# Kernel tuning notes

Measured on AMD Instinct MI355X. Metric: run time of the kernel, lower is better.

## Reference

```python
import jax, jax.numpy as jnp
import numpy as np

ATT = 512  # attention_size

def setup_inputs() -> dict:
    key = jax.random.key(0)
    k0, k1, k2, k3, k4 = jax.random.split(key, 5)
    B, Sq, Sk, Din, Dmem = 32, 1024, 1024, 512, 512
    inputs = jax.random.normal(k0, (B, Sq, Din), dtype=jnp.float32)
    memory = jax.random.normal(k1, (B, Sk, Dmem), dtype=jnp.float32)
    memory_mask = jax.random.randint(k2, (B, Sk), 0, 2).astype(jnp.int32)
    W_input = (jax.random.normal(k3, (Din, ATT), dtype=jnp.float32) * 0.02)
    W_memory = (jax.random.normal(k4, (Dmem, ATT), dtype=jnp.float32) * 0.02)
    return {"inputs": inputs, "memory": memory, "memory_mask": memory_mask,
            "W_input": W_input, "W_memory": W_memory}

def reference(inputs, memory, memory_mask, W_input, W_memory):
    # projections (bias=False) + ReLU; dropout=0 -> identity
    x = jax.nn.relu(jnp.einsum('bqd,da->bqa', inputs, W_input))   # [B,Sq,A]
    m = jax.nn.relu(jnp.einsum('bkd,da->bka', memory, W_memory))  # [B,Sk,A]
    scale = 1.0 / jnp.sqrt(jnp.asarray(ATT, dtype=inputs.dtype))
    logits = jnp.einsum('bqa,bka->bqk', x, m) * scale             # [B,Sq,Sk]
    mask = (memory_mask[:, None, :] != 0)                         # [B,1,Sk] broadcast over Sq
    logits = jnp.where(mask, logits, jnp.asarray(-1e30, dtype=logits.dtype))
    score = jax.nn.softmax(logits, axis=-1)
    context = jnp.einsum('bqk,bkd->bqd', score, memory)           # [B,Sq,Dmem]
    return jnp.concatenate([context, inputs], axis=-1)            # [B,Sq,Dmem+Din]
```

## Files before the change

### kernel.cpp

```cpp
#include <hip/hip_runtime.h>

typedef __bf16 bf16x8 __attribute__((ext_vector_type(8)));
typedef float f32x4 __attribute__((ext_vector_type(4)));

__device__ __forceinline__ unsigned short f2bf(float f) {
    union { float f; unsigned u; } v; v.f = f;
    unsigned r = v.u + 0x7FFFu + ((v.u >> 16) & 1u);
    return (unsigned short)(r >> 16);
}

__global__ __launch_bounds__(256) void transpose_to_bf16(
    const float* __restrict__ src, unsigned short* __restrict__ dst,
    unsigned short* __restrict__ dst_copy, int S, int D)
{
    __shared__ float tile[32][33];
    const float* sb = src + (size_t)blockIdx.z * S * D;
    unsigned short* db = dst + (size_t)blockIdx.z * S * D;
    const int s0 = blockIdx.x * 32, d0 = blockIdx.y * 32;
    const int t = threadIdx.x;
    const int tr = t >> 5, tc = t & 31;
#pragma unroll
    for (int i = 0; i < 4; i++) {
        int s = s0 + tr + i * 8;
        float v = sb[(size_t)s * D + d0 + tc];
        tile[tr + i * 8][tc] = v;
        if (dst_copy)
            dst_copy[(size_t)blockIdx.z * S * D + (size_t)s * D + d0 + tc] = f2bf(v);
    }
    __syncthreads();
#pragma unroll
    for (int i = 0; i < 4; i++) {
        int d = d0 + tr + i * 8;
        db[(size_t)d * S + s0 + tc] = f2bf(tile[tc][tr + i * 8]);
    }
}

__global__ __launch_bounds__(256) void fuse_inputs_kernel(
    const float4* __restrict__ in, uint2* __restrict__ in_bf16, float4* __restrict__ out)
{
    int i = blockIdx.x * 256 + threadIdx.x;
    int bq = i >> 7;
    int d  = i & 127;
    float4 v = in[i];
    out[(size_t)bq * 256 + 128 + d] = v;
    union { unsigned short u[4]; uint2 p; } pk;
    pk.u[0] = f2bf(v.x); pk.u[1] = f2bf(v.y);
    pk.u[2] = f2bf(v.z); pk.u[3] = f2bf(v.w);
    in_bf16[i] = pk.p;
}

template<int CMODE>
__global__ __launch_bounds__(256, 2) void gemm_bt(
    const unsigned short* __restrict__ A, const unsigned short* __restrict__ Bt,
    void* __restrict__ Cptr, int K, float scale,
    const int* __restrict__ maskp, float* __restrict__ rowsum,
    long long aStride, long long bStride, long long cStride, int ldc)
{
    __shared__ __align__(16) unsigned short As[128 * 32];
    __shared__ __align__(16) unsigned short Bs[128 * 32];

    const int t = threadIdx.x;
    const int lane = t & 63;
    const int wave = t >> 6;
    const int z = blockIdx.z;

    const unsigned short* Ab = A + (size_t)z * aStride;
    const unsigned short* Bb = Bt + (size_t)z * bStride;

    const int rowA = blockIdx.y * 128;
    const int rowB = blockIdx.x * 128;

    f32x4 acc[4][4];
#pragma unroll
    for (int i = 0; i < 4; i++)
#pragma unroll
        for (int j = 0; j < 4; j++) acc[i][j] = f32x4{0.f, 0.f, 0.f, 0.f};

    const int wm = (wave >> 1) * 64;
    const int wn = (wave & 1) * 64;
    const int lrow = lane & 15;
    const int lk = (lane >> 4) * 8;

    const int sr = lane >> 2;
    const int skk = (lane & 3) * 8;
    const int c0 = wave, c1 = wave + 4;

    for (int kt = 0; kt < K; kt += 32) {
        const unsigned short* gb0 = Bb + (size_t)(rowB + c0 * 16 + sr) * K + kt + skk;
        const unsigned short* gb1 = Bb + (size_t)(rowB + c1 * 16 + sr) * K + kt + skk;
        __builtin_amdgcn_global_load_lds((const __attribute__((address_space(1))) void*)gb0,
                                         (__attribute__((address_space(3))) void*)&Bs[c0 * 512], 16, 0, 0);
        __builtin_amdgcn_global_load_lds((const __attribute__((address_space(1))) void*)gb1,
                                         (__attribute__((address_space(3))) void*)&Bs[c1 * 512], 16, 0, 0);
        const unsigned short* ga0 = Ab + (size_t)(rowA + c0 * 16 + sr) * K + kt + skk;
        const unsigned short* ga1 = Ab + (size_t)(rowA + c1 * 16 + sr) * K + kt + skk;
        __builtin_amdgcn_global_load_lds((const __attribute__((address_space(1))) void*)ga0,
                                         (__attribute__((address_space(3))) void*)&As[c0 * 512], 16, 0, 0);
        __builtin_amdgcn_global_load_lds((const __attribute__((address_space(1))) void*)ga1,
                                         (__attribute__((address_space(3))) void*)&As[c1 * 512], 16, 0, 0);
        __syncthreads();

        bf16x8 a[4], b[4];
#pragma unroll
        for (int i = 0; i < 4; i++) a[i] = *(const bf16x8*)&As[(wm + i * 16 + lrow) * 32 + lk];
#pragma unroll
        for (int j = 0; j < 4; j++) b[j] = *(const bf16x8*)&Bs[(wn + j * 16 + lrow) * 32 + lk];
#pragma unroll
        for (int i = 0; i < 4; i++)
#pragma unroll
            for (int j = 0; j < 4; j++)
                acc[i][j] = __builtin_amdgcn_mfma_f32_16x16x32_bf16(a[i], b[j], acc[i][j], 0, 0, 0);
        __syncthreads();
    }

    const int orow = (lane >> 4) * 4;
    const int ocol = lane & 15;

    if constexpr (CMODE == 0) {
        unsigned short* C = (unsigned short*)Cptr + (size_t)z * cStride;
#pragma unroll
        for (int i = 0; i < 4; i++)
#pragma unroll
            for (int j = 0; j < 4; j++) {
                int col = rowB + wn + j * 16 + ocol;
#pragma unroll
                for (int r = 0; r < 4; r++) {
                    int rw = rowA + wm + i * 16 + orow + r;
                    C[(size_t)rw * ldc + col] = f2bf(fmaxf(acc[i][j][r], 0.f));
                }
            }
    } else if constexpr (CMODE == 1) {
        unsigned short* C = (unsigned short*)Cptr + (size_t)z * cStride;
        const int* mk = maskp + (size_t)z * 1024;
        float* rs = rowsum + (size_t)z * 1024;
        int mv[4];
#pragma unroll
        for (int j = 0; j < 4; j++) mv[j] = mk[rowB + wn + j * 16 + ocol];
#pragma unroll
        for (int i = 0; i < 4; i++) {
            float part[4] = {0.f, 0.f, 0.f, 0.f};
#pragma unroll
            for (int j = 0; j < 4; j++) {
                int col = rowB + wn + j * 16 + ocol;
#pragma unroll
                for (int r = 0; r < 4; r++) {
                    float p = mv[j] ? __expf(acc[i][j][r] * scale) : 0.f;
                    part[r] += p;
                    int rw = rowA + wm + i * 16 + orow + r;
                    C[(size_t)rw * ldc + col] = f2bf(p);
                }
            }
#pragma unroll
            for (int r = 0; r < 4; r++) {
                float s = part[r];
                s += __shfl_xor(s, 1, 64);
                s += __shfl_xor(s, 2, 64);
                s += __shfl_xor(s, 4, 64);
                s += __shfl_xor(s, 8, 64);
                if (ocol == 0) atomicAdd(&rs[rowA + wm + i * 16 + orow + r], s);
            }
        }
    } else {
        float* C = (float*)Cptr + (size_t)z * cStride;
        const float* rs = rowsum + (size_t)z * 1024;
#pragma unroll
        for (int i = 0; i < 4; i++) {
            float inv[4];
#pragma unroll
            for (int r = 0; r < 4; r++)
                inv[r] = 1.0f / rs[rowA + wm + i * 16 + orow + r];
#pragma unroll
            for (int j = 0; j < 4; j++) {
                int col = rowB + wn + j * 16 + ocol;
#pragma unroll
                for (int r = 0; r < 4; r++) {
                    int rw = rowA + wm + i * 16 + orow + r;
                    C[(size_t)rw * ldc + col] = acc[i][j][r] * inv[r];
                }
            }
        }
    }
}

extern "C" void kernel_launch(void* const* d_in, const int* in_sizes, int n_in,
                              void* d_out, int out_size, void* d_ws, size_t ws_size,
                              hipStream_t stream)
{
    const float* inputs = (const float*)d_in[0];
    const float* memory = (const float*)d_in[1];
    const int*   mmask  = (const int*)d_in[2];
    const float* W_in   = (const float*)d_in[3];
    const float* W_mem  = (const float*)d_in[4];
    float* out = (float*)d_out;

    char* ws = (char*)d_ws;
    const unsigned long long MB = 1048576ull;
    unsigned short* Wt_in  = (unsigned short*)(ws);
    unsigned short* Wt_mem = (unsigned short*)(ws + 524288);
    unsigned short* InB16  = (unsigned short*)(ws + 1 * MB);
    unsigned short* MemB16 = (unsigned short*)(ws + 1 * MB + 32 * MB);
    unsigned short* P      = (unsigned short*)(ws + 1 * MB);
    unsigned short* MemT   = (unsigned short*)(ws + 1 * MB + 64 * MB);
    unsigned short* Xq     = (unsigned short*)(ws + 1 * MB + 96 * MB);
    unsigned short* Xm     = (unsigned short*)(ws + 1 * MB + 128 * MB);
    float*          rowsum = (float*)(ws + 1 * MB + 160 * MB);

    const float scale = 0.04419417382415922f;

    transpose_to_bf16<<<dim3(16, 16, 1), 256, 0, stream>>>(W_in,  Wt_in,  nullptr, 512, 512);
    transpose_to_bf16<<<dim3(16, 16, 1), 256, 0, stream>>>(W_mem, Wt_mem, nullptr, 512, 512);
    transpose_to_bf16<<<dim3(32, 16, 32), 256, 0, stream>>>(memory, MemT, MemB16, 1024, 512);

    fuse_inputs_kernel<<<16384, 256, 0, stream>>>(
        (const float4*)inputs, (uint2*)InB16, (float4*)out);

    hipMemsetAsync(rowsum, 0, 32 * 1024 * sizeof(float), stream);

    gemm_bt<0><<<dim3(4, 256, 1), 256, 0, stream>>>(
        InB16, Wt_in, Xq, 512, 0.f, nullptr, nullptr, 0, 0, 0, 512);
    gemm_bt<0><<<dim3(4, 256, 1), 256, 0, stream>>>(
        MemB16, Wt_mem, Xm, 512, 0.f, nullptr, nullptr, 0, 0, 0, 512);

    gemm_bt<1><<<dim3(8, 8, 32), 256, 0, stream>>>(
        Xq, Xm, P, 512, scale, mmask, rowsum, 1024ll * 512, 1024ll * 512, 1024ll * 1024, 1024);

    gemm_bt<2><<<dim3(4, 8, 32), 256, 0, stream>>>(
        P, MemT, out, 1024, 1.f, nullptr, rowsum, 1024ll * 1024, 512ll * 1024, 1024ll * 1024, 1024);
}
```

Before: 454.2 us.

## Compact unmasked memory keys and skip masked work in attention GEMMs

Adds a per-batch prefix scan over the memory mask that builds a compacted list of valid key indices and a count padded to 128. Memory rows are gathered into compacted bf16 and transposed buffers, so the memory projection, the QK logits GEMM and the PV GEMM only cover the valid keys, with early exits for tiles past the padded count and a dynamic K in the final GEMM. About half the keys are masked, so roughly half the attention and memory-projection FLOPs go away. The cost is an extra scan launch and a gather with indirect reads.

```diff
diff --git a/kernel.cpp b/kernel.cpp
--- a/kernel.cpp
+++ b/kernel.cpp
@@ -9,29 +9,82 @@
     return (unsigned short)(r >> 16);
 }
 
-__global__ __launch_bounds__(256) void transpose_to_bf16(
-    const float* __restrict__ src, unsigned short* __restrict__ dst,
-    unsigned short* __restrict__ dst_copy, int S, int D)
+__global__ __launch_bounds__(256) void mask_scan_kernel(
+    const int* __restrict__ mask, int* __restrict__ kidx,
+    int* __restrict__ cnt, int* __restrict__ padded)
+{
+    const int b = blockIdx.x;
+    const int* m = mask + b * 1024;
+    const int t = threadIdx.x;
+    int v[4]; int s = 0;
+#pragma unroll
+    for (int e = 0; e < 4; e++) { v[e] = (m[t * 4 + e] != 0) ? 1 : 0; s += v[e]; }
+    const int lane = t & 63, wv = t >> 6;
+    int x = s;
+#pragma unroll
+    for (int off = 1; off < 64; off <<= 1) {
+        int y = __shfl_up(x, off, 64);
+        if (lane >= off) x += y;
+    }
+    __shared__ int wsum[4];
+    if (lane == 63) wsum[wv] = x;
+    __syncthreads();
+    int base = 0;
+    for (int w = 0; w < wv; w++) base += wsum[w];
+    int pos = base + x - s;
+#pragma unroll
+    for (int e = 0; e < 4; e++)
+        if (v[e]) kidx[b * 1024 + pos++] = t * 4 + e;
+    if (t == 255) {
+        int total = base + x;
+        cnt[b] = total;
+        padded[b] = (total + 127) & ~127;
+    }
+}
+
+__global__ __launch_bounds__(256) void transpose_w_kernel(
+    const float* __restrict__ W0, const float* __restrict__ W1,
+    unsigned short* __restrict__ D0, unsigned short* __restrict__ D1)
 {
     __shared__ float tile[32][33];
-    const float* sb = src + (size_t)blockIdx.z * S * D;
-    unsigned short* db = dst + (size_t)blockIdx.z * S * D;
+    const float* src = blockIdx.z ? W1 : W0;
+    unsigned short* dst = blockIdx.z ? D1 : D0;
     const int s0 = blockIdx.x * 32, d0 = blockIdx.y * 32;
-    const int t = threadIdx.x;
-    const int tr = t >> 5, tc = t & 31;
+    const int t = threadIdx.x, tr = t >> 5, tc = t & 31;
+#pragma unroll
+    for (int i = 0; i < 4; i++)
+        tile[tr + i * 8][tc] = src[(size_t)(s0 + tr + i * 8) * 512 + d0 + tc];
+    __syncthreads();
+#pragma unroll
+    for (int i = 0; i < 4; i++)
+        dst[(size_t)(d0 + tr + i * 8) * 512 + s0 + tc] = f2bf(tile[tc][tr + i * 8]);
+}
+
+__global__ __launch_bounds__(256) void gather_mem_kernel(
+    const float* __restrict__ memory, const int* __restrict__ kidx,
+    const int* __restrict__ cnt, const int* __restrict__ padded,
+    unsigned short* __restrict__ MemG, unsigned short* __restrict__ MemGT)
+{
+    const int b = blockIdx.z;
+    const int j0 = blockIdx.x * 32, d0 = blockIdx.y * 32;
+    if (j0 >= padded[b]) return;
+    const int nb = cnt[b];
+    __shared__ float tile[32][33];
+    const float* src = memory + (size_t)b * 1024 * 512;
+    const int t = threadIdx.x, tr = t >> 5, tc = t & 31;
 #pragma unroll
     for (int i = 0; i < 4; i++) {
-        int s = s0 + tr + i * 8;
-        float v = sb[(size_t)s * D + d0 + tc];
+        int j = j0 + tr + i * 8;
+        float v = 0.f;
+        if (j < nb) v = src[(size_t)kidx[b * 1024 + j] * 512 + d0 + tc];
         tile[tr + i * 8][tc] = v;
-        if (dst_copy)
-            dst_copy[(size_t)blockIdx.z * S * D + (size_t)s * D + d0 + tc] = f2bf(v);
+        MemG[(size_t)b * 1024 * 512 + (size_t)j * 512 + d0 + tc] = f2bf(v);
     }
     __syncthreads();
 #pragma unroll
     for (int i = 0; i < 4; i++) {
         int d = d0 + tr + i * 8;
-        db[(size_t)d * S + s0 + tc] = f2bf(tile[tc][tr + i * 8]);
+        MemGT[(size_t)b * 512 * 1024 + (size_t)d * 1024 + j0 + tc] = f2bf(tile[tc][tr + i * 8]);
     }
 }
 
@@ -49,26 +102,30 @@
     in_bf16[i] = pk.p;
 }
 
-template<int CMODE>
+template<int CMODE, int LIMA, int LIMB, int KDYN>
 __global__ __launch_bounds__(256, 2) void gemm_bt(
     const unsigned short* __restrict__ A, const unsigned short* __restrict__ Bt,
-    void* __restrict__ Cptr, int K, float scale,
-    const int* __restrict__ maskp, float* __restrict__ rowsum,
+    void* __restrict__ Cptr, int K, int lda, int ldb, float scale,
+    const int* __restrict__ cnt, const int* __restrict__ padded,
+    float* __restrict__ rowsum,
     long long aStride, long long bStride, long long cStride, int ldc)
 {
+    const int z = blockIdx.z;
+    const int rowA = blockIdx.y * 128;
+    const int rowB = blockIdx.x * 128;
+    if (LIMA && rowA >= padded[z]) return;
+    if (LIMB && rowB >= padded[z]) return;
+    const int Kz = KDYN ? padded[z] : K;
+
     __shared__ __align__(16) unsigned short As[128 * 32];
     __shared__ __align__(16) unsigned short Bs[128 * 32];
 
     const int t = threadIdx.x;
     const int lane = t & 63;
     const int wave = t >> 6;
-    const int z = blockIdx.z;
 
     const unsigned short* Ab = A + (size_t)z * aStride;
     const unsigned short* Bb = Bt + (size_t)z * bStride;
-
-    const int rowA = blockIdx.y * 128;
-    const int rowB = blockIdx.x * 128;
 
     f32x4 acc[4][4];
 #pragma unroll
@@ -85,15 +142,15 @@
     const int skk = (lane & 3) * 8;
     const int c0 = wave, c1 = wave + 4;
 
-    for (int kt = 0; kt < K; kt += 32) {
-        const unsigned short* gb0 = Bb + (size_t)(rowB + c0 * 16 + sr) * K + kt + skk;
-        const unsigned short* gb1 = Bb + (size_t)(rowB + c1 * 16 + sr) * K + kt + skk;
+    for (int kt = 0; kt < Kz; kt += 32) {
+        const unsigned short* gb0 = Bb + (size_t)(rowB + c0 * 16 + sr) * ldb + kt + skk;
+        const unsigned short* gb1 = Bb + (size_t)(rowB + c1 * 16 + sr) * ldb + kt + skk;
         __builtin_amdgcn_global_load_lds((const __attribute__((address_space(1))) void*)gb0,
                                          (__attribute__((address_space(3))) void*)&Bs[c0 * 512], 16, 0, 0);
         __builtin_amdgcn_global_load_lds((const __attribute__((address_space(1))) void*)gb1,
                                          (__attribute__((address_space(3))) void*)&Bs[c1 * 512], 16, 0, 0);
-        const unsigned short* ga0 = Ab + (size_t)(rowA + c0 * 16 + sr) * K + kt + skk;
-        const unsigned short* ga1 = Ab + (size_t)(rowA + c1 * 16 + sr) * K + kt + skk;
+        const unsigned short* ga0 = Ab + (size_t)(rowA + c0 * 16 + sr) * lda + kt + skk;
+        const unsigned short* ga1 = Ab + (size_t)(rowA + c1 * 16 + sr) * lda + kt + skk;
         __builtin_amdgcn_global_load_lds((const __attribute__((address_space(1))) void*)ga0,
                                          (__attribute__((address_space(3))) void*)&As[c0 * 512], 16, 0, 0);
         __builtin_amdgcn_global_load_lds((const __attribute__((address_space(1))) void*)ga1,
@@ -131,11 +188,8 @@
             }
     } else if constexpr (CMODE == 1) {
         unsigned short* C = (unsigned short*)Cptr + (size_t)z * cStride;
-        const int* mk = maskp + (size_t)z * 1024;
+        const int nb = cnt[z];
         float* rs = rowsum + (size_t)z * 1024;
-        int mv[4];
-#pragma unroll
-        for (int j = 0; j < 4; j++) mv[j] = mk[rowB + wn + j * 16 + ocol];
 #pragma unroll
         for (int i = 0; i < 4; i++) {
             float part[4] = {0.f, 0.f, 0.f, 0.f};
@@ -144,7 +198,7 @@
                 int col = rowB + wn + j * 16 + ocol;
 #pragma unroll
                 for (int r = 0; r < 4; r++) {
-                    float p = mv[j] ? __expf(acc[i][j][r] * scale) : 0.f;
+                    float p = (col < nb) ? __expf(acc[i][j][r] * scale) : 0.f;
                     part[r] += p;
                     int rw = rowA + wm + i * 16 + orow + r;
                     C[(size_t)rw * ldc + col] = f2bf(p);
@@ -198,32 +252,41 @@
     unsigned short* Wt_in  = (unsigned short*)(ws);
     unsigned short* Wt_mem = (unsigned short*)(ws + 524288);
     unsigned short* InB16  = (unsigned short*)(ws + 1 * MB);
-    unsigned short* MemB16 = (unsigned short*)(ws + 1 * MB + 32 * MB);
+    unsigned short* MemG   = (unsigned short*)(ws + 33 * MB);
     unsigned short* P      = (unsigned short*)(ws + 1 * MB);
-    unsigned short* MemT   = (unsigned short*)(ws + 1 * MB + 64 * MB);
-    unsigned short* Xq     = (unsigned short*)(ws + 1 * MB + 96 * MB);
-    unsigned short* Xm     = (unsigned short*)(ws + 1 * MB + 128 * MB);
-    float*          rowsum = (float*)(ws + 1 * MB + 160 * MB);
+    unsigned short* MemGT  = (unsigned short*)(ws + 65 * MB);
+    unsigned short* Xq     = (unsigned short*)(ws + 97 * MB);
+    unsigned short* Xm     = (unsigned short*)(ws + 129 * MB);
+    float*          rowsum = (float*)(ws + 161 * MB);
+    int*            kidx   = (int*)(ws + 161 * MB + 131072);
+    int*            cntp   = (int*)(ws + 161 * MB + 262144);
+    int*            padp   = (int*)(ws + 161 * MB + 262144 + 128);
 
     const float scale = 0.04419417382415922f;
 
-    transpose_to_bf16<<<dim3(16, 16, 1), 256, 0, stream>>>(W_in,  Wt_in,  nullptr, 512, 512);
-    transpose_to_bf16<<<dim3(16, 16, 1), 256, 0, stream>>>(W_mem, Wt_mem, nullptr, 512, 512);
-    transpose_to_bf16<<<dim3(32, 16, 32), 256, 0, stream>>>(memory, MemT, MemB16, 1024, 512);
+    mask_scan_kernel<<<32, 256, 0, stream>>>(mmask, kidx, cntp, padp);
+    transpose_w_kernel<<<dim3(16, 16, 2), 256, 0, stream>>>(W_in, W_mem, Wt_in, Wt_mem);
+
+    gather_mem_kernel<<<dim3(32, 16, 32), 256, 0, stream>>>(
+        memory, kidx, cntp, padp, MemG, MemGT);
 
     fuse_inputs_kernel<<<16384, 256, 0, stream>>>(
         (const float4*)inputs, (uint2*)InB16, (float4*)out);
 
     hipMemsetAsync(rowsum, 0, 32 * 1024 * sizeof(float), stream);
 
-    gemm_bt<0><<<dim3(4, 256, 1), 256, 0, stream>>>(
-        InB16, Wt_in, Xq, 512, 0.f, nullptr, nullptr, 0, 0, 0, 512);
-    gemm_bt<0><<<dim3(4, 256, 1), 256, 0, stream>>>(
-        MemB16, Wt_mem, Xm, 512, 0.f, nullptr, nullptr, 0, 0, 0, 512);
-
-    gemm_bt<1><<<dim3(8, 8, 32), 256, 0, stream>>>(
-        Xq, Xm, P, 512, scale, mmask, rowsum, 1024ll * 512, 1024ll * 512, 1024ll * 1024, 1024);
-
-    gemm_bt<2><<<dim3(4, 8, 32), 256, 0, stream>>>(
-        P, MemT, out, 1024, 1.f, nullptr, rowsum, 1024ll * 1024, 512ll * 1024, 1024ll * 1024, 1024);
-}
+    gemm_bt<0, 0, 0, 0><<<dim3(4, 256, 1), 256, 0, stream>>>(
+        InB16, Wt_in, Xq, 512, 512, 512, 0.f, nullptr, nullptr, nullptr,
+        0, 0, 0, 512);
+    gemm_bt<0, 1, 0, 0><<<dim3(4, 8, 32), 256, 0, stream>>>(
+        MemG, Wt_mem, Xm, 512, 512, 512, 0.f, nullptr, padp, nullptr,
+        1024ll * 512, 0, 1024ll * 512, 512);
+
+    gemm_bt<1, 0, 1, 0><<<dim3(8, 8, 32), 256, 0, stream>>>(
+        Xq, Xm, P, 512, 512, 512, scale, cntp, padp, rowsum,
+        1024ll * 512, 1024ll * 512, 1024ll * 1024, 1024);
+
+    gemm_bt<2, 0, 0, 1><<<dim3(4, 8, 32), 256, 0, stream>>>(
+        P, MemGT, out, 1024, 1024, 1024, 1.f, nullptr, padp, rowsum,
+        1024ll * 1024, 512ll * 1024, 1024ll * 1024, 1024);
+}
```

Result: faster. 438.1 us (-3.6%).
